# Kernel tuning notes

Hardware: AMD Instinct MI355X
Metric: run time of the kernel (lower is better)

The kernel has to match this reference:

```python
import jax, jax.numpy as jnp
import numpy as np

N = 100000   # vertices
T = 128      # temporal depth
E = 1600000  # edges (avg degree 16)
K = 9        # conv kernel size
PAD = 4      # 'same' padding -> T preserved
L = 3        # number of layers


def setup_inputs() -> dict:
    key = jax.random.key(0)
    ks = jax.random.split(key, 6)
    x = jax.random.normal(ks[0], (N, T), dtype=jnp.float32)
    edge_index = jax.random.randint(ks[1], (2, E), 0, N, dtype=jnp.int32)
    conv_w = jax.random.normal(ks[2], (L, 1, 1, K), dtype=jnp.float32) * (1.0 / np.sqrt(K))
    conv_b = jax.random.normal(ks[3], (L, 1), dtype=jnp.float32) * 0.1
    W_out = jax.random.normal(ks[4], (3, N), dtype=jnp.float32) * (1.0 / np.sqrt(N))
    b_out = jax.random.normal(ks[5], (3,), dtype=jnp.float32) * 0.1
    return {"x": x, "edge_index": edge_index, "conv_w": conv_w,
            "conv_b": conv_b, "W_out": W_out, "b_out": b_out}


def _conv1d(x, w, b):
    # x: [N, T], w: [1, 1, K] (OIH), b: [1]; torch Conv1d = cross-correlation.
    y = jax.lax.conv_general_dilated(
        x[:, None, :], w, window_strides=(1,), padding=[(PAD, PAD)],
        dimension_numbers=("NCH", "OIH", "NCH"))
    return y[:, 0, :] + b  # [N, T]


def reference(x, edge_index, conv_w, conv_b, W_out, b_out):
    # add_self_loops: append (i, i) for every node
    loop = jnp.arange(N, dtype=edge_index.dtype)
    src = jnp.concatenate([edge_index[0], loop])  # message sources
    dst = jnp.concatenate([edge_index[1], loop])  # aggregation targets
    # in-degree counts (>=1 due to self loops) for mean aggregation
    cnt = jax.ops.segment_sum(jnp.ones(src.shape, jnp.float32), dst,
                              num_segments=N)[:, None]  # [N, 1]
    for i in range(L):
        h = _conv1d(x, conv_w[i], conv_b[i])                    # [N, T]
        s = jax.ops.segment_sum(h[src], dst, num_segments=N)    # scatter-sum of gathered msgs
        x = jax.nn.relu(s / cnt)                                # mean aggr + relu
    x = x.reshape(-1, N)            # [T, N] (row-major view like torch .view)
    return x @ W_out.T + b_out      # [T, 3]
```

## Files before the change

### kernel.cpp

```cpp
#include <hip/hip_runtime.h>

#define NN 100000
#define TT 128
#define EE 1600000
#define KK 9
#define PADK 4
#define NSPLIT 8

#define BSH 9
#define BMASK 511
#define NBUCK 196
#define BCAP 10240

typedef _Float16 f16;
typedef __attribute__((ext_vector_type(2))) _Float16 f16x2;
typedef __attribute__((ext_vector_type(4))) _Float16 f16x4;

__global__ void bin_kernel(const int* __restrict__ ei, int* __restrict__ gcursor,
                           unsigned int* __restrict__ binned) {
    __shared__ int hist[NBUCK];
    __shared__ int gbase[NBUCK];
    int tid = threadIdx.x;
    for (int i = tid; i < NBUCK; i += 256) hist[i] = 0;
    __syncthreads();
    int base = blockIdx.x * 2048;
    unsigned int val[8];
    int bkt[8];
    int rank[8];
#pragma unroll
    for (int k = 0; k < 8; k++) {
        int e = base + k * 256 + tid;
        bkt[k] = -1;
        if (e < EE) {
            int s = ei[e];
            int d = ei[EE + e];
            bkt[k] = d >> BSH;
            val[k] = ((unsigned int)(d & BMASK) << 20) | (unsigned int)s;
            rank[k] = atomicAdd(&hist[bkt[k]], 1);
        }
    }
    __syncthreads();
    for (int i = tid; i < NBUCK; i += 256)
        gbase[i] = hist[i] ? atomicAdd(&gcursor[i], hist[i]) : 0;
    __syncthreads();
#pragma unroll
    for (int k = 0; k < 8; k++) {
        if (bkt[k] >= 0)
            binned[(size_t)bkt[k] * BCAP + gbase[bkt[k]] + rank[k]] = val[k];
    }
}

__global__ void scanpart_kernel(const int* __restrict__ gcursor, int* __restrict__ part,
                                int* __restrict__ offsets) {
    __shared__ int sm[256];
    int tid = threadIdx.x;
    sm[tid] = (tid < NBUCK) ? gcursor[tid] : 0;
    __syncthreads();
    for (int off = 1; off < 256; off <<= 1) {
        int v = (tid >= off) ? sm[tid - off] : 0;
        __syncthreads();
        sm[tid] += v;
        __syncthreads();
    }
    if (tid < NBUCK) part[tid] = (tid == 0) ? 0 : sm[tid - 1];
    if (tid == 0) offsets[NN] = EE;
}

__global__ void bucket_csr_kernel(const unsigned int* __restrict__ binned,
                                  const int* __restrict__ gcursor,
                                  const int* __restrict__ part,
                                  int* __restrict__ offsets,
                                  float* __restrict__ inv_cnt,
                                  int* __restrict__ col) {
    __shared__ int hist[512];
    __shared__ int cur[512];
    __shared__ int sm[256];
    int b = blockIdx.x;
    int tid = threadIdx.x;
    int cnt = gcursor[b];
    const unsigned int* ePtr = binned + (size_t)b * BCAP;
    hist[tid] = 0;
    hist[tid + 256] = 0;
    __syncthreads();
    for (int j = tid; j < cnt; j += 256)
        atomicAdd(&hist[ePtr[j] >> 20], 1);
    __syncthreads();
    int d0 = hist[2 * tid], d1 = hist[2 * tid + 1];
    sm[tid] = d0 + d1;
    __syncthreads();
    for (int off = 1; off < 256; off <<= 1) {
        int v = (tid >= off) ? sm[tid - off] : 0;
        __syncthreads();
        sm[tid] += v;
        __syncthreads();
    }
    int basep = part[b] + ((tid == 0) ? 0 : sm[tid - 1]);
    int node0 = (b << BSH) + 2 * tid;
    int p0 = basep;
    int p1 = basep + d0;
    if (node0 < NN) {
        offsets[node0] = p0;
        inv_cnt[node0] = 1.0f / (1.0f + (float)d0);
        cur[2 * tid] = p0;
    }
    if (node0 + 1 < NN) {
        offsets[node0 + 1] = p1;
        inv_cnt[node0 + 1] = 1.0f / (1.0f + (float)d1);
        cur[2 * tid + 1] = p1;
    }
    __syncthreads();
    for (int j = tid; j < cnt; j += 256) {
        unsigned int v = ePtr[j];
        int pos = atomicAdd(&cur[v >> 20], 1);
        col[pos] = (int)(v & 0xFFFFF);
    }
}

__global__ void cvt_kernel(const float4* __restrict__ x, f16x4* __restrict__ x16) {
    int i = blockIdx.x * blockDim.x + threadIdx.x;
    float4 v = x[i];
    f16x4 o;
    o.x = (f16)v.x; o.y = (f16)v.y; o.z = (f16)v.z; o.w = (f16)v.w;
    x16[i] = o;
}

__global__ void fused_layer_kernel(const f16x2* __restrict__ xin,
                                   const int* __restrict__ offsets,
                                   const int* __restrict__ col,
                                   const float* __restrict__ inv_cnt,
                                   const float* __restrict__ w9,
                                   const float* __restrict__ bptr,
                                   f16x2* __restrict__ yout) {
    int tid = threadIdx.x;
    int lane = tid & 63;
    int node = blockIdx.x * 4 + (tid >> 6);

    f16x2 sv = xin[node * 64 + lane];
    float ax = (float)sv.x;
    float ay = (float)sv.y;

    int lo = offsets[node], hi = offsets[node + 1];
    int cnt = hi - lo;
    int my_col = (lane < cnt) ? col[lo + lane] : 0;
    int jn = cnt < 64 ? cnt : 64;
    int j = 0;
    for (; j + 3 < jn; j += 4) {
        int c0 = __shfl(my_col, j);
        int c1 = __shfl(my_col, j + 1);
        int c2 = __shfl(my_col, j + 2);
        int c3 = __shfl(my_col, j + 3);
        f16x2 v0 = xin[c0 * 64 + lane];
        f16x2 v1 = xin[c1 * 64 + lane];
        f16x2 v2 = xin[c2 * 64 + lane];
        f16x2 v3 = xin[c3 * 64 + lane];
        ax += (float)v0.x + (float)v1.x + (float)v2.x + (float)v3.x;
        ay += (float)v0.y + (float)v1.y + (float)v2.y + (float)v3.y;
    }
    for (; j < jn; j++) {
        int c = __shfl(my_col, j);
        f16x2 v = xin[c * 64 + lane];
        ax += (float)v.x;
        ay += (float)v.y;
    }
    for (int k = 64; k < cnt; k++) {
        int c = col[lo + k];
        f16x2 v = xin[c * 64 + lane];
        ax += (float)v.x;
        ay += (float)v.y;
    }

    float u1x = __shfl_up(ax, 1), u1y = __shfl_up(ay, 1);
    float u2x = __shfl_up(ax, 2), u2y = __shfl_up(ay, 2);
    float d1x = __shfl_down(ax, 1), d1y = __shfl_down(ay, 1);
    float d2x = __shfl_down(ax, 2), d2y = __shfl_down(ay, 2);
    if (lane < 1) { u1x = 0.0f; u1y = 0.0f; }
    if (lane < 2) { u2x = 0.0f; u2y = 0.0f; }
    if (lane > 62) { d1x = 0.0f; d1y = 0.0f; }
    if (lane > 61) { d2x = 0.0f; d2y = 0.0f; }

    float w0 = w9[0], w1 = w9[1], w2 = w9[2], w3 = w9[3], w4 = w9[4];
    float w5 = w9[5], w6 = w9[6], w7 = w9[7], w8 = w9[8];
    float s0 = u2x * w0 + u2y * w1 + u1x * w2 + u1y * w3 + ax * w4
             + ay * w5 + d1x * w6 + d1y * w7 + d2x * w8;
    float s1 = u2y * w0 + u1x * w1 + u1y * w2 + ax * w3 + ay * w4
             + d1x * w5 + d1y * w6 + d2x * w7 + d2y * w8;

    float ic = inv_cnt[node];
    float b = bptr[0];
    s0 = fmaxf(s0 * ic + b, 0.0f);
    s1 = fmaxf(s1 * ic + b, 0.0f);
    f16x2 o;
    o.x = (f16)s0;
    o.y = (f16)s1;
    yout[node * 64 + lane] = o;
}

__global__ void out_kernel(const f16* __restrict__ y3, const float* __restrict__ Wout,
                           const float* __restrict__ bout, float* __restrict__ out) {
    int t = blockIdx.x;
    int sp = blockIdx.y;
    int tid = threadIdx.x;
    const int per = NN / NSPLIT;
    int lo = sp * per;
    int hi = lo + per;
    float a0 = 0.0f, a1 = 0.0f, a2 = 0.0f;
    for (int n = lo + tid * 2; n < hi; n += 512) {
        f16x2 v2 = *(const f16x2*)(y3 + (size_t)t * NN + n);
        float vx = (float)v2.x, vy = (float)v2.y;
        float2 wA = *(const float2*)(Wout + n);
        float2 wB = *(const float2*)(Wout + NN + n);
        float2 wC = *(const float2*)(Wout + 2 * NN + n);
        a0 += vx * wA.x + vy * wA.y;
        a1 += vx * wB.x + vy * wB.y;
        a2 += vx * wC.x + vy * wC.y;
    }
    for (int o = 32; o > 0; o >>= 1) {
        a0 += __shfl_down(a0, o);
        a1 += __shfl_down(a1, o);
        a2 += __shfl_down(a2, o);
    }
    __shared__ float red[4][3];
    int wave = tid >> 6;
    if ((tid & 63) == 0) {
        red[wave][0] = a0;
        red[wave][1] = a1;
        red[wave][2] = a2;
    }
    __syncthreads();
    if (tid == 0) {
        float r0 = red[0][0] + red[1][0] + red[2][0] + red[3][0];
        float r1 = red[0][1] + red[1][1] + red[2][1] + red[3][1];
        float r2 = red[0][2] + red[1][2] + red[2][2] + red[3][2];
        if (sp == 0) {
            r0 += bout[0];
            r1 += bout[1];
            r2 += bout[2];
        }
        atomicAdd(&out[t * 3 + 0], r0);
        atomicAdd(&out[t * 3 + 1], r1);
        atomicAdd(&out[t * 3 + 2], r2);
    }
}

extern "C" void kernel_launch(void* const* d_in, const int* in_sizes, int n_in,
                              void* d_out, int out_size, void* d_ws, size_t ws_size,
                              hipStream_t stream) {
    const float* x    = (const float*)d_in[0];
    const int*   ei   = (const int*)d_in[1];
    const float* cw   = (const float*)d_in[2];
    const float* cb   = (const float*)d_in[3];
    const float* Wout = (const float*)d_in[4];
    const float* bout = (const float*)d_in[5];
    float* out = (float*)d_out;

    char* ws = (char*)d_ws;
    size_t off = 0;
    auto alloc = [&](size_t bytes) -> void* {
        void* p = ws + off;
        off += (bytes + 255) & ~(size_t)255;
        return p;
    };
    f16*          x16     = (f16*)alloc((size_t)NN * TT * 2);
    f16*          yA      = (f16*)alloc((size_t)NN * TT * 2);
    f16*          yB      = (f16*)alloc((size_t)NN * TT * 2);
    unsigned int* binned  = (unsigned int*)alloc((size_t)NBUCK * BCAP * 4);
    int*          gcursor = (int*)alloc((size_t)NBUCK * 4);
    int*          part    = (int*)alloc((size_t)NBUCK * 4);
    int*          offsets = (int*)alloc((size_t)(NN + 1) * 4);
    float*        inv_cnt = (float*)alloc((size_t)NN * 4);
    int*          col     = (int*)alloc((size_t)EE * 4);

    hipMemsetAsync(gcursor, 0, (size_t)NBUCK * 4, stream);
    bin_kernel<<<(EE + 2047) / 2048, 256, 0, stream>>>(ei, gcursor, binned);
    scanpart_kernel<<<1, 256, 0, stream>>>(gcursor, part, offsets);
    bucket_csr_kernel<<<NBUCK, 256, 0, stream>>>(binned, gcursor, part, offsets, inv_cnt, col);

    cvt_kernel<<<(NN * TT / 4 + 255) / 256, 256, 0, stream>>>((const float4*)x, (f16x4*)x16);

    fused_layer_kernel<<<NN / 4, 256, 0, stream>>>((const f16x2*)x16, offsets, col, inv_cnt,
                                                   cw + 0 * KK, cb + 0, (f16x2*)yA);
    fused_layer_kernel<<<NN / 4, 256, 0, stream>>>((const f16x2*)yA, offsets, col, inv_cnt,
                                                   cw + 1 * KK, cb + 1, (f16x2*)yB);
    fused_layer_kernel<<<NN / 4, 256, 0, stream>>>((const f16x2*)yB, offsets, col, inv_cnt,
                                                   cw + 2 * KK, cb + 2, (f16x2*)yA);

    hipMemsetAsync(out, 0, (size_t)TT * 3 * 4, stream);
    out_kernel<<<dim3(TT, NSPLIT), 256, 0, stream>>>(yA, Wout, bout, out);
}
```

Measured before the change: 358.5 us.

## Split each wave into two half-waves gathering separate neighbours with packed fp16 accumulation

Each 64-lane wave now treats a node's 128-step row as 32 lanes of 4 fp16 values, so the two half-waves gather different neighbour rows at the same time and combine them with a cross-half xor shuffle. Neighbour sums accumulate in packed fp16 vectors instead of fp32 scalars, which cuts the conversion ALU work and doubles the bytes per load. The 9-tap conv is rebuilt from width-4 windows plus one-lane shifts. The cost is reduced precision, since up to roughly 16 or more fp16 values are summed before conversion to fp32, and the upper half-wave sits idle on the store.

After: 366.6 us. 1.02x slower.

```diff
diff --git a/kernel.cpp b/kernel.cpp
--- a/kernel.cpp
+++ b/kernel.cpp
@@ -15,6 +15,8 @@
 typedef _Float16 f16;
 typedef __attribute__((ext_vector_type(2))) _Float16 f16x2;
 typedef __attribute__((ext_vector_type(4))) _Float16 f16x4;
+
+union HU { f16x4 h; int2 i; };
 
 __global__ void bin_kernel(const int* __restrict__ ei, int* __restrict__ gcursor,
                            unsigned int* __restrict__ binned) {
@@ -124,75 +126,91 @@
     x16[i] = o;
 }
 
-__global__ void fused_layer_kernel(const f16x2* __restrict__ xin,
+__global__ void fused_layer_kernel(const f16x4* __restrict__ xin,
                                    const int* __restrict__ offsets,
                                    const int* __restrict__ col,
                                    const float* __restrict__ inv_cnt,
                                    const float* __restrict__ w9,
                                    const float* __restrict__ bptr,
-                                   f16x2* __restrict__ yout) {
+                                   f16x4* __restrict__ yout) {
     int tid = threadIdx.x;
     int lane = tid & 63;
+    int half = lane >> 5;
+    int p = lane & 31;
     int node = blockIdx.x * 4 + (tid >> 6);
-
-    f16x2 sv = xin[node * 64 + lane];
-    float ax = (float)sv.x;
-    float ay = (float)sv.y;
 
     int lo = offsets[node], hi = offsets[node + 1];
     int cnt = hi - lo;
     int my_col = (lane < cnt) ? col[lo + lane] : 0;
     int jn = cnt < 64 ? cnt : 64;
+
+    const f16 z = (f16)0;
+    const f16 hm = half ? (f16)0 : (f16)1;
+    f16x4 hmask = {hm, hm, hm, hm};
+    f16x4 acc0 = {z, z, z, z};
+    f16x4 acc1 = {z, z, z, z};
+
     int j = 0;
     for (; j + 3 < jn; j += 4) {
-        int c0 = __shfl(my_col, j);
-        int c1 = __shfl(my_col, j + 1);
-        int c2 = __shfl(my_col, j + 2);
-        int c3 = __shfl(my_col, j + 3);
-        f16x2 v0 = xin[c0 * 64 + lane];
-        f16x2 v1 = xin[c1 * 64 + lane];
-        f16x2 v2 = xin[c2 * 64 + lane];
-        f16x2 v3 = xin[c3 * 64 + lane];
-        ax += (float)v0.x + (float)v1.x + (float)v2.x + (float)v3.x;
-        ay += (float)v0.y + (float)v1.y + (float)v2.y + (float)v3.y;
-    }
-    for (; j < jn; j++) {
+        int c0 = __shfl(my_col, j + half);
+        int c1 = __shfl(my_col, j + 2 + half);
+        f16x4 v0 = xin[(c0 << 5) | p];
+        f16x4 v1 = xin[(c1 << 5) | p];
+        acc0 += v0;
+        acc1 += v1;
+    }
+    for (; j + 1 < jn; j += 2) {
+        int c = __shfl(my_col, j + half);
+        acc0 += xin[(c << 5) | p];
+    }
+    if (j < jn) {
         int c = __shfl(my_col, j);
-        f16x2 v = xin[c * 64 + lane];
-        ax += (float)v.x;
-        ay += (float)v.y;
+        acc1 += xin[(c << 5) | p] * hmask;
     }
     for (int k = 64; k < cnt; k++) {
         int c = col[lo + k];
-        f16x2 v = xin[c * 64 + lane];
-        ax += (float)v.x;
-        ay += (float)v.y;
-    }
-
-    float u1x = __shfl_up(ax, 1), u1y = __shfl_up(ay, 1);
-    float u2x = __shfl_up(ax, 2), u2y = __shfl_up(ay, 2);
-    float d1x = __shfl_down(ax, 1), d1y = __shfl_down(ay, 1);
-    float d2x = __shfl_down(ax, 2), d2y = __shfl_down(ay, 2);
-    if (lane < 1) { u1x = 0.0f; u1y = 0.0f; }
-    if (lane < 2) { u2x = 0.0f; u2y = 0.0f; }
-    if (lane > 62) { d1x = 0.0f; d1y = 0.0f; }
-    if (lane > 61) { d2x = 0.0f; d2y = 0.0f; }
+        acc0 += xin[(c << 5) | p] * hmask;
+    }
+    acc0 += acc1;
+
+    HU u; u.h = acc0;
+    int2 o2;
+    o2.x = __shfl_xor(u.i.x, 32);
+    o2.y = __shfl_xor(u.i.y, 32);
+    HU w; w.i = o2;
+    acc0 += w.h;
+
+    f16x4 sv = xin[(node << 5) | p];
+    float a0 = (float)acc0.x + (float)sv.x;
+    float a1 = (float)acc0.y + (float)sv.y;
+    float a2 = (float)acc0.z + (float)sv.z;
+    float a3 = (float)acc0.w + (float)sv.w;
+
+    float p0 = __shfl_up(a0, 1, 32), p1 = __shfl_up(a1, 1, 32);
+    float p2 = __shfl_up(a2, 1, 32), p3 = __shfl_up(a3, 1, 32);
+    float n0 = __shfl_down(a0, 1, 32), n1 = __shfl_down(a1, 1, 32);
+    float n2 = __shfl_down(a2, 1, 32), n3 = __shfl_down(a3, 1, 32);
+    if (p == 0)  { p0 = 0.0f; p1 = 0.0f; p2 = 0.0f; p3 = 0.0f; }
+    if (p == 31) { n0 = 0.0f; n1 = 0.0f; n2 = 0.0f; n3 = 0.0f; }
 
     float w0 = w9[0], w1 = w9[1], w2 = w9[2], w3 = w9[3], w4 = w9[4];
     float w5 = w9[5], w6 = w9[6], w7 = w9[7], w8 = w9[8];
-    float s0 = u2x * w0 + u2y * w1 + u1x * w2 + u1y * w3 + ax * w4
-             + ay * w5 + d1x * w6 + d1y * w7 + d2x * w8;
-    float s1 = u2y * w0 + u1x * w1 + u1y * w2 + ax * w3 + ay * w4
-             + d1x * w5 + d1y * w6 + d2x * w7 + d2y * w8;
+    float s0 = p0*w0 + p1*w1 + p2*w2 + p3*w3 + a0*w4 + a1*w5 + a2*w6 + a3*w7 + n0*w8;
+    float s1 = p1*w0 + p2*w1 + p3*w2 + a0*w3 + a1*w4 + a2*w5 + a3*w6 + n0*w7 + n1*w8;
+    float s2 = p2*w0 + p3*w1 + a0*w2 + a1*w3 + a2*w4 + a3*w5 + n0*w6 + n1*w7 + n2*w8;
+    float s3 = p3*w0 + a0*w1 + a1*w2 + a2*w3 + a3*w4 + n0*w5 + n1*w6 + n2*w7 + n3*w8;
 
     float ic = inv_cnt[node];
     float b = bptr[0];
     s0 = fmaxf(s0 * ic + b, 0.0f);
     s1 = fmaxf(s1 * ic + b, 0.0f);
-    f16x2 o;
-    o.x = (f16)s0;
-    o.y = (f16)s1;
-    yout[node * 64 + lane] = o;
+    s2 = fmaxf(s2 * ic + b, 0.0f);
+    s3 = fmaxf(s3 * ic + b, 0.0f);
+    if (half == 0) {
+        f16x4 o;
+        o.x = (f16)s0; o.y = (f16)s1; o.z = (f16)s2; o.w = (f16)s3;
+        yout[(node << 5) | p] = o;
+    }
 }
 
 __global__ void out_kernel(const f16* __restrict__ y3, const float* __restrict__ Wout,
@@ -277,12 +295,12 @@
 
     cvt_kernel<<<(NN * TT / 4 + 255) / 256, 256, 0, stream>>>((const float4*)x, (f16x4*)x16);
 
-    fused_layer_kernel<<<NN / 4, 256, 0, stream>>>((const f16x2*)x16, offsets, col, inv_cnt,
-                                                   cw + 0 * KK, cb + 0, (f16x2*)yA);
-    fused_layer_kernel<<<NN / 4, 256, 0, stream>>>((const f16x2*)yA, offsets, col, inv_cnt,
-                                                   cw + 1 * KK, cb + 1, (f16x2*)yB);
-    fused_layer_kernel<<<NN / 4, 256, 0, stream>>>((const f16x2*)yB, offsets, col, inv_cnt,
-                                                   cw + 2 * KK, cb + 2, (f16x2*)yA);
+    fused_layer_kernel<<<NN / 4, 256, 0, stream>>>((const f16x4*)x16, offsets, col, inv_cnt,
+                                                   cw + 0 * KK, cb + 0, (f16x4*)yA);
+    fused_layer_kernel<<<NN / 4, 256, 0, stream>>>((const f16x4*)yA, offsets, col, inv_cnt,
+                                                   cw + 1 * KK, cb + 1, (f16x4*)yB);
+    fused_layer_kernel<<<NN / 4, 256, 0, stream>>>((const f16x4*)yB, offsets, col, inv_cnt,
+                                                   cw + 2 * KK, cb + 2, (f16x4*)yA);
 
     hipMemsetAsync(out, 0, (size_t)TT * 3 * 4, stream);
     out_kernel<<<dim3(TT, NSPLIT), 256, 0, stream>>>(yA, Wout, bout, out);
```
